# Performance work log

Hardware: AMD Instinct MI355X
Metric: run time of the kernel (lower is better)

The kernel has to match this reference:

```python
import jax, jax.numpy as jnp
import numpy as np

N_NODES = 100000
N_EDGES = 1600000
D_FEAT = 50
N_CLASSES = 47
K_HOPS = 2


def setup_inputs() -> dict:
    key = jax.random.key(0)
    k1, k2, k3, k4 = jax.random.split(key, 4)
    feat = jax.random.normal(k1, (N_NODES, D_FEAT), dtype=jnp.float32)
    edge_src = jax.random.randint(k2, (N_EDGES,), 0, N_NODES)
    edge_dst = jax.random.randint(k3, (N_EDGES,), 0, N_NODES)
    # xavier_uniform for fc.weight [n_classes, in_feats], zeros bias
    limit = np.sqrt(6.0 / (N_CLASSES + D_FEAT)).astype(np.float32)
    W = jax.random.uniform(k4, (N_CLASSES, D_FEAT), dtype=jnp.float32,
                           minval=-limit, maxval=limit)
    b = jnp.zeros((N_CLASSES,), dtype=jnp.float32)
    return {"feat": feat, "W": W, "b": b,
            "edge_src": edge_src, "edge_dst": edge_dst, "K": K_HOPS}


def reference(feat, W, b, edge_src, edge_dst, K):
    # S = D^-1/2 (A + I) D^-1/2 ; precompute = S^K ; out = (S^K feat) W^T + b
    N = feat.shape[0]
    ones = jnp.ones_like(edge_dst, dtype=feat.dtype)
    deg = 1.0 + jax.ops.segment_sum(ones, edge_dst, num_segments=N)  # row sums of A+I
    dinv = jax.lax.rsqrt(deg)                       # [N]
    w_e = dinv[edge_dst] * dinv[edge_src]           # [E] edge weights of S
    self_w = dinv * dinv                            # [N] self-loop weights (1/d)
    h = feat
    for _ in range(K):  # K hops: h <- S @ h
        msg = w_e[:, None] * h[edge_src]            # [E, D] gather + scale
        h = jax.ops.segment_sum(msg, edge_dst, num_segments=N) + self_w[:, None] * h
    return h @ W.T + b                              # [N, n_classes]
```

## Files before the change

### kernel.cpp

```cpp
#include <hip/hip_runtime.h>
#include <hip/hip_fp16.h>

#define NN 100000
#define NE 1600000
#define DF 50
#define NC 47
#define DP 64
#define ZROW NN
#define MAXDEG 48

#define RB   128
#define RSH  7
#define RNG  782
#define CCH  250
#define CI4  (NE / 4 / CCH)
#define BK   48

static_assert(NN % 16 == 0, "grid exactness");
static_assert((NE / 4) % CCH == 0, "chunk exactness");

typedef _Float16 half8 __attribute__((ext_vector_type(8)));
typedef float float4v __attribute__((ext_vector_type(4)));
typedef int int4v __attribute__((ext_vector_type(4)));

__global__ __launch_bounds__(256) void binA_kernel(const int4v* __restrict__ src4,
                                                   const int4v* __restrict__ dst4,
                                                   unsigned* __restrict__ arena,
                                                   unsigned short* __restrict__ counts) {
    __shared__ unsigned lcnt[RNG];
    int c = blockIdx.x;
    for (int i = threadIdx.x; i < RNG; i += 256) lcnt[i] = 0;
    __syncthreads();
    int base = c * CI4;
    for (int i = threadIdx.x; i < CI4; i += 256) {
        int4v s = __builtin_nontemporal_load(&src4[base + i]);
        int4v q = __builtin_nontemporal_load(&dst4[base + i]);
        #pragma unroll
        for (int k = 0; k < 4; ++k) {
            unsigned d  = (unsigned)q[k];
            unsigned r  = d >> RSH;
            unsigned dl = d & (RB - 1);
            unsigned p  = atomicAdd(&lcnt[r], 1u);
            if (p < BK)
                arena[((size_t)r * CCH + c) * BK + p] = (unsigned)s[k] | (dl << 17);
        }
    }
    __syncthreads();
    for (int i = threadIdx.x; i < RNG; i += 256)
        counts[(size_t)c * RNG + i] = (unsigned short)min(lcnt[i], (unsigned)BK);
}

__global__ __launch_bounds__(256) void slotB_kernel(const unsigned* __restrict__ arena,
                                                    const unsigned short* __restrict__ counts,
                                                    int* __restrict__ cols,
                                                    unsigned* __restrict__ deg) {
    __shared__ unsigned lcur[RB];
    int r = blockIdx.x;
    if (threadIdx.x < RB) lcur[threadIdx.x] = 0;
    __syncthreads();
    int c = threadIdx.x;
    if (c < CCH) {
        int cnt = counts[(size_t)c * RNG + r];
        const unsigned* bk = arena + ((size_t)r * CCH + c) * BK;
        for (int j = 0; j < cnt; ++j) {
            unsigned e    = bk[j];
            unsigned srcv = e & 0x1FFFFu;
            unsigned dl   = (e >> 17) & (RB - 1);
            unsigned p    = atomicAdd(&lcur[dl], 1u);
            if (p < MAXDEG)
                cols[((size_t)r * RB + dl) * MAXDEG + p] = (int)srcv;
        }
    }
    __syncthreads();
    if (threadIdx.x < RB) {
        int node = r * RB + threadIdx.x;
        if (node < NN) deg[node] = lcur[threadIdx.x];
    }
}

__global__ void pad_kernel(const unsigned* __restrict__ deg, const float* __restrict__ f,
                           float* __restrict__ dinv, float* __restrict__ selfw,
                           float4* __restrict__ fp, float4* __restrict__ h1p4) {
    int t = blockIdx.x * blockDim.x + threadIdx.x;
    if (t >= (NN + 1) * 8) return;
    int n = t >> 3, c = t & 7;
    float r = 0.f;
    if (n < NN) r = rsqrtf(1.0f + (float)deg[n]);
    if (c == 0 && n < NN) {
        dinv[n]  = r;
        selfw[n] = r * r;
    }
    float v[8];
    #pragma unroll
    for (int i = 0; i < 8; ++i) {
        int e = c * 8 + i;
        v[i] = (n < NN && e < DF) ? r * f[n * DF + e] : 0.f;
    }
    float4 ov;
    __half2* op = (__half2*)&ov;
    #pragma unroll
    for (int i = 0; i < 4; ++i) op[i] = __floats2half2_rn(v[2 * i], v[2 * i + 1]);
    fp[t] = ov;
    if (n == NN) h1p4[t] = make_float4(0.f, 0.f, 0.f, 0.f);
}

__global__ __launch_bounds__(256) void hop_kernel(const _Float16* __restrict__ h,
    const int* __restrict__ cols, const unsigned* __restrict__ deg,
    const float* __restrict__ scaleArr, _Float16* __restrict__ hn) {

    int lane = threadIdx.x & 63;
    int wid  = (int)((blockIdx.x * blockDim.x + threadIdx.x) >> 6);
    int half = lane >> 5;
    int g    = (lane >> 3) & 3;
    int qid  = lane & 7;

    int nd = 2 * wid + half;
    unsigned rs = (unsigned)nd * MAXDEG;
    unsigned d  = min(deg[nd], (unsigned)MAXDEG);
    unsigned dmax = max(__shfl(d, 0), __shfl(d, 32));

    float acc[8] = {0.f, 0.f, 0.f, 0.f, 0.f, 0.f, 0.f, 0.f};

    auto body = [&](unsigned j) {
        int c = __builtin_nontemporal_load(&cols[rs + j]);
        c = (j < d) ? c : ZROW;
        half8 v = *(const half8*)(h + (unsigned)c * DP + qid * 8);
        #pragma unroll
        for (int i = 0; i < 8; ++i) acc[i] += (float)v[i];
    };

    for (unsigned j0 = 0; j0 < dmax; j0 += 32u) {
        #pragma unroll
        for (int u = 0; u < 4; ++u) body(j0 + (unsigned)(g + 4 * u));
        if (j0 + 16u < dmax) {
            #pragma unroll
            for (int u = 4; u < 8; ++u) body(j0 + (unsigned)(g + 4 * u));
        }
    }

    #pragma unroll
    for (int i = 0; i < 8; ++i) {
        acc[i] += __shfl_xor(acc[i], 8);
        acc[i] += __shfl_xor(acc[i], 16);
    }

    float s = scaleArr[nd];
    half8 hv = *(const half8*)(h + (unsigned)nd * DP + qid * 8);
    half8 ov;
    #pragma unroll
    for (int i = 0; i < 8; ++i)
        ov[i] = (_Float16)(s * (acc[i] + (float)hv[i]));
    if ((lane & 24) == 0)
        __builtin_nontemporal_store(ov, (half8*)(hn + (unsigned)nd * DP + qid * 8));
}

__global__ __launch_bounds__(256) void fc_kernel(const _Float16* __restrict__ h2,
    const float* __restrict__ W, const float* __restrict__ b,
    float* __restrict__ out, int MT) {

    __shared__ _Float16 sW[48 * 72];
    __shared__ float sB[48];

    for (int i = threadIdx.x; i < 48 * 64; i += 256) {
        int n = i >> 6, k = i & 63;
        float v = (n < NC && k < DF) ? W[n * DF + k] : 0.f;
        sW[n * 72 + k] = (_Float16)v;
    }
    if (threadIdx.x < 48) sB[threadIdx.x] = (threadIdx.x < NC) ? b[threadIdx.x] : 0.f;
    __syncthreads();

    int lane = threadIdx.x & 63;
    int wid  = (int)((blockIdx.x * blockDim.x + threadIdx.x) >> 6);
    if (wid >= MT) return;

    int m0 = wid * 16;
    int am = lane & 15;
    int aq = lane >> 4;

    const half8* arow = (const half8*)(h2 + (long)(m0 + am) * DP);
    half8 a0 = arow[aq];
    half8 a1 = arow[aq + 4];
    int row = aq * 4;

    #pragma unroll
    for (int t = 0; t < 3; ++t) {
        int n = t * 16 + am;
        const half8* brow = (const half8*)(sW + n * 72);
        half8 b0 = brow[aq];
        half8 b1 = brow[aq + 4];
        float4v c = {0.f, 0.f, 0.f, 0.f};
        c = __builtin_amdgcn_mfma_f32_16x16x32_f16(a0, b0, c, 0, 0, 0);
        c = __builtin_amdgcn_mfma_f32_16x16x32_f16(a1, b1, c, 0, 0, 0);
        if (n < NC) {
            float bn = sB[n];
            #pragma unroll
            for (int r = 0; r < 4; ++r)
                out[(long)(m0 + row + r) * NC + n] = c[r] + bn;
        }
    }
}

extern "C" void kernel_launch(void* const* d_in, const int* in_sizes, int n_in,
                              void* d_out, int out_size, void* d_ws, size_t ws_size,
                              hipStream_t stream) {
    const float* feat = (const float*)d_in[0];
    const float* W    = (const float*)d_in[1];
    const float* b    = (const float*)d_in[2];
    const int*  esrc  = (const int*)d_in[3];
    const int*  edst  = (const int*)d_in[4];
    float* out = (float*)d_out;

    char* ws = (char*)d_ws;
    unsigned* deg    = (unsigned*)ws;       ws += ((size_t)NN * 4 + 127) & ~127ull;
    float*    dinv   = (float*)ws;          ws += ((size_t)NN * 4 + 127) & ~127ull;
    float*    selfw  = (float*)ws;          ws += ((size_t)NN * 4 + 127) & ~127ull;
    int*      cols   = (int*)ws;            ws += ((size_t)NN * MAXDEG * 4 + 127) & ~127ull;
    unsigned short* counts = (unsigned short*)ws; ws += ((size_t)CCH * RNG * 2 + 127) & ~127ull;
    char* uni = ws;
    unsigned* arena  = (unsigned*)uni;
    _Float16* featp  = (_Float16*)uni;
    _Float16* h1p    = featp + (size_t)(NN + 1) * DP;
    _Float16* h2p    = h1p   + (size_t)(NN + 1) * DP;

    binA_kernel<<<CCH, 256, 0, stream>>>((const int4v*)esrc, (const int4v*)edst, arena, counts);
    slotB_kernel<<<RNG, 256, 0, stream>>>(arena, counts, cols, deg);

    pad_kernel<<<((NN + 1) * 8 + 255) / 256, 256, 0, stream>>>(
        deg, feat, dinv, selfw, (float4*)featp, (float4*)h1p);

    const int hop_blocks = NN / 8;
    hop_kernel<<<hop_blocks, 256, 0, stream>>>(featp, cols, deg, selfw, h1p);
    hop_kernel<<<hop_blocks, 256, 0, stream>>>(h1p, cols, deg, dinv, h2p);

    const int MT = NN / 16;
    fc_kernel<<<(MT + 3) / 4, 256, 0, stream>>>(h2p, W, b, out, MT);
}
```

Before: 220.8 us.

## Apply linear layer before propagation and fuse bias into final hop

Reorders the computation to (S^K X W^T) so the dense projection runs first on raw features, folding the dinv scaling and padding into the projection kernel. The second hop now writes the final fp32 output with bias directly, which removes the separate pad and fc kernels and the h2 intermediate buffer. The binning stage also doubles the chunk count and halves the per-bucket capacity, which changes the parallelism of the edge-binning pass. Risks are fp16 rounding of the projected features and bucket overflow, which silently drops edges, now that the per-bucket cap is smaller.

After: 223.7 us. About the same (+1.3%).

```diff
diff --git a/kernel.cpp b/kernel.cpp
--- a/kernel.cpp
+++ b/kernel.cpp
@@ -12,9 +12,9 @@
 #define RB   128
 #define RSH  7
 #define RNG  782
-#define CCH  250
+#define CCH  500
 #define CI4  (NE / 4 / CCH)
-#define BK   48
+#define BK   24
 
 static_assert(NN % 16 == 0, "grid exactness");
 static_assert((NE / 4) % CCH == 0, "chunk exactness");
@@ -58,8 +58,7 @@
     int r = blockIdx.x;
     if (threadIdx.x < RB) lcur[threadIdx.x] = 0;
     __syncthreads();
-    int c = threadIdx.x;
-    if (c < CCH) {
+    for (int c = threadIdx.x; c < CCH; c += 256) {
         int cnt = counts[(size_t)c * RNG + r];
         const unsigned* bk = arena + ((size_t)r * CCH + c) * BK;
         for (int j = 0; j < cnt; ++j) {
@@ -78,109 +77,50 @@
     }
 }
 
-__global__ void pad_kernel(const unsigned* __restrict__ deg, const float* __restrict__ f,
-                           float* __restrict__ dinv, float* __restrict__ selfw,
-                           float4* __restrict__ fp, float4* __restrict__ h1p4) {
-    int t = blockIdx.x * blockDim.x + threadIdx.x;
-    if (t >= (NN + 1) * 8) return;
-    int n = t >> 3, c = t & 7;
-    float r = 0.f;
-    if (n < NN) r = rsqrtf(1.0f + (float)deg[n]);
-    if (c == 0 && n < NN) {
-        dinv[n]  = r;
-        selfw[n] = r * r;
-    }
-    float v[8];
-    #pragma unroll
-    for (int i = 0; i < 8; ++i) {
-        int e = c * 8 + i;
-        v[i] = (n < NN && e < DF) ? r * f[n * DF + e] : 0.f;
-    }
-    float4 ov;
-    __half2* op = (__half2*)&ov;
-    #pragma unroll
-    for (int i = 0; i < 4; ++i) op[i] = __floats2half2_rn(v[2 * i], v[2 * i + 1]);
-    fp[t] = ov;
-    if (n == NN) h1p4[t] = make_float4(0.f, 0.f, 0.f, 0.f);
-}
-
-__global__ __launch_bounds__(256) void hop_kernel(const _Float16* __restrict__ h,
-    const int* __restrict__ cols, const unsigned* __restrict__ deg,
-    const float* __restrict__ scaleArr, _Float16* __restrict__ hn) {
-
-    int lane = threadIdx.x & 63;
-    int wid  = (int)((blockIdx.x * blockDim.x + threadIdx.x) >> 6);
-    int half = lane >> 5;
-    int g    = (lane >> 3) & 3;
-    int qid  = lane & 7;
-
-    int nd = 2 * wid + half;
-    unsigned rs = (unsigned)nd * MAXDEG;
-    unsigned d  = min(deg[nd], (unsigned)MAXDEG);
-    unsigned dmax = max(__shfl(d, 0), __shfl(d, 32));
-
-    float acc[8] = {0.f, 0.f, 0.f, 0.f, 0.f, 0.f, 0.f, 0.f};
-
-    auto body = [&](unsigned j) {
-        int c = __builtin_nontemporal_load(&cols[rs + j]);
-        c = (j < d) ? c : ZROW;
-        half8 v = *(const half8*)(h + (unsigned)c * DP + qid * 8);
-        #pragma unroll
-        for (int i = 0; i < 8; ++i) acc[i] += (float)v[i];
-    };
-
-    for (unsigned j0 = 0; j0 < dmax; j0 += 32u) {
-        #pragma unroll
-        for (int u = 0; u < 4; ++u) body(j0 + (unsigned)(g + 4 * u));
-        if (j0 + 16u < dmax) {
-            #pragma unroll
-            for (int u = 4; u < 8; ++u) body(j0 + (unsigned)(g + 4 * u));
-        }
-    }
-
-    #pragma unroll
-    for (int i = 0; i < 8; ++i) {
-        acc[i] += __shfl_xor(acc[i], 8);
-        acc[i] += __shfl_xor(acc[i], 16);
-    }
-
-    float s = scaleArr[nd];
-    half8 hv = *(const half8*)(h + (unsigned)nd * DP + qid * 8);
-    half8 ov;
-    #pragma unroll
-    for (int i = 0; i < 8; ++i)
-        ov[i] = (_Float16)(s * (acc[i] + (float)hv[i]));
-    if ((lane & 24) == 0)
-        __builtin_nontemporal_store(ov, (half8*)(hn + (unsigned)nd * DP + qid * 8));
-}
-
-__global__ __launch_bounds__(256) void fc_kernel(const _Float16* __restrict__ h2,
-    const float* __restrict__ W, const float* __restrict__ b,
-    float* __restrict__ out, int MT) {
-
+__global__ __launch_bounds__(256) void yw_kernel(const float* __restrict__ feat,
+                                                 const unsigned* __restrict__ deg,
+                                                 const float* __restrict__ W,
+                                                 _Float16* __restrict__ Y,
+                                                 _Float16* __restrict__ h1p, int MT) {
     __shared__ _Float16 sW[48 * 72];
-    __shared__ float sB[48];
+    __shared__ _Float16 sY[4][16][72];
 
     for (int i = threadIdx.x; i < 48 * 64; i += 256) {
         int n = i >> 6, k = i & 63;
         float v = (n < NC && k < DF) ? W[n * DF + k] : 0.f;
         sW[n * 72 + k] = (_Float16)v;
     }
-    if (threadIdx.x < 48) sB[threadIdx.x] = (threadIdx.x < NC) ? b[threadIdx.x] : 0.f;
     __syncthreads();
 
     int lane = threadIdx.x & 63;
-    int wid  = (int)((blockIdx.x * blockDim.x + threadIdx.x) >> 6);
-    if (wid >= MT) return;
+    int w    = threadIdx.x >> 6;
+    int wid  = blockIdx.x * 4 + w;
+    if (wid > MT) return;
+    if (wid == MT) {
+        half8 z = {};
+        if (lane < 8)       *(half8*)(Y   + (size_t)ZROW * DP + lane * 8) = z;
+        else if (lane < 16) *(half8*)(h1p + (size_t)ZROW * DP + (lane - 8) * 8) = z;
+        return;
+    }
 
     int m0 = wid * 16;
     int am = lane & 15;
     int aq = lane >> 4;
-
-    const half8* arow = (const half8*)(h2 + (long)(m0 + am) * DP);
-    half8 a0 = arow[aq];
-    half8 a1 = arow[aq + 4];
     int row = aq * 4;
+
+    const float* arow = feat + (size_t)(m0 + am) * DF;
+    half8 a0, a1;
+    #pragma unroll
+    for (int j = 0; j < 8; ++j) {
+        a0[j] = (_Float16)arow[aq * 8 + j];
+        int k1 = 32 + aq * 8 + j;
+        a1[j] = (k1 < DF) ? (_Float16)arow[k1] : (_Float16)0.f;
+    }
+
+    float dv[4];
+    #pragma unroll
+    for (int r = 0; r < 4; ++r)
+        dv[r] = rsqrtf(1.0f + (float)deg[m0 + row + r]);
 
     #pragma unroll
     for (int t = 0; t < 3; ++t) {
@@ -191,11 +131,103 @@
         float4v c = {0.f, 0.f, 0.f, 0.f};
         c = __builtin_amdgcn_mfma_f32_16x16x32_f16(a0, b0, c, 0, 0, 0);
         c = __builtin_amdgcn_mfma_f32_16x16x32_f16(a1, b1, c, 0, 0, 0);
-        if (n < NC) {
-            float bn = sB[n];
+        #pragma unroll
+        for (int r = 0; r < 4; ++r)
+            sY[w][row + r][n] = (_Float16)(c[r] * dv[r]);
+    }
+    #pragma unroll
+    for (int r = 0; r < 4; ++r)
+        sY[w][row + r][48 + am] = (_Float16)0.f;
+
+    int row2 = lane >> 2, q = lane & 3;
+    half8 y0 = *(half8*)&sY[w][row2][q * 16];
+    half8 y1 = *(half8*)&sY[w][row2][q * 16 + 8];
+    _Float16* orow = Y + (size_t)(m0 + row2) * DP + q * 16;
+    *(half8*)orow = y0;
+    *(half8*)(orow + 8) = y1;
+}
+
+__device__ __forceinline__ void gather_sum(const _Float16* __restrict__ h,
+    const int* __restrict__ cols, unsigned rs, unsigned d, unsigned dmax,
+    int qid, int g, float* acc) {
+    auto body = [&](unsigned j) {
+        int c = __builtin_nontemporal_load(&cols[rs + j]);
+        c = (j < d) ? c : ZROW;
+        half8 v = *(const half8*)(h + (unsigned)c * DP + qid * 8);
+        #pragma unroll
+        for (int i = 0; i < 8; ++i) acc[i] += (float)v[i];
+    };
+    for (unsigned j0 = 0; j0 < dmax; j0 += 32u) {
+        #pragma unroll
+        for (int u = 0; u < 4; ++u) body(j0 + (unsigned)(g + 4 * u));
+        if (j0 + 16u < dmax) {
             #pragma unroll
-            for (int r = 0; r < 4; ++r)
-                out[(long)(m0 + row + r) * NC + n] = c[r] + bn;
+            for (int u = 4; u < 8; ++u) body(j0 + (unsigned)(g + 4 * u));
+        }
+    }
+    #pragma unroll
+    for (int i = 0; i < 8; ++i) {
+        acc[i] += __shfl_xor(acc[i], 8);
+        acc[i] += __shfl_xor(acc[i], 16);
+    }
+}
+
+__global__ __launch_bounds__(256) void hop1_kernel(const _Float16* __restrict__ h,
+    const int* __restrict__ cols, const unsigned* __restrict__ deg,
+    _Float16* __restrict__ hn) {
+
+    int lane = threadIdx.x & 63;
+    int wid  = (int)((blockIdx.x * blockDim.x + threadIdx.x) >> 6);
+    int half = lane >> 5, g = (lane >> 3) & 3, qid = lane & 7;
+
+    int nd = 2 * wid + half;
+    unsigned du = deg[nd];
+    unsigned d  = min(du, (unsigned)MAXDEG);
+    unsigned dmax = max(__shfl(d, 0), __shfl(d, 32));
+    unsigned rs = (unsigned)nd * MAXDEG;
+
+    float acc[8] = {0.f, 0.f, 0.f, 0.f, 0.f, 0.f, 0.f, 0.f};
+    gather_sum(h, cols, rs, d, dmax, qid, g, acc);
+
+    float s = 1.0f / (1.0f + (float)du);
+    half8 hv = *(const half8*)(h + (unsigned)nd * DP + qid * 8);
+    half8 ov;
+    #pragma unroll
+    for (int i = 0; i < 8; ++i)
+        ov[i] = (_Float16)(s * (acc[i] + (float)hv[i]));
+    if ((lane & 24) == 0)
+        __builtin_nontemporal_store(ov, (half8*)(hn + (unsigned)nd * DP + qid * 8));
+}
+
+__global__ __launch_bounds__(256) void hop2_kernel(const _Float16* __restrict__ h,
+    const int* __restrict__ cols, const unsigned* __restrict__ deg,
+    const float* __restrict__ bias, float* __restrict__ out) {
+
+    __shared__ float sB[64];
+    if (threadIdx.x < 64) sB[threadIdx.x] = (threadIdx.x < NC) ? bias[threadIdx.x] : 0.f;
+    __syncthreads();
+
+    int lane = threadIdx.x & 63;
+    int wid  = (int)((blockIdx.x * blockDim.x + threadIdx.x) >> 6);
+    int half = lane >> 5, g = (lane >> 3) & 3, qid = lane & 7;
+
+    int nd = 2 * wid + half;
+    unsigned du = deg[nd];
+    unsigned d  = min(du, (unsigned)MAXDEG);
+    unsigned dmax = max(__shfl(d, 0), __shfl(d, 32));
+    unsigned rs = (unsigned)nd * MAXDEG;
+
+    float acc[8] = {0.f, 0.f, 0.f, 0.f, 0.f, 0.f, 0.f, 0.f};
+    gather_sum(h, cols, rs, d, dmax, qid, g, acc);
+
+    float s = rsqrtf(1.0f + (float)du);
+    half8 hv = *(const half8*)(h + (unsigned)nd * DP + qid * 8);
+    if ((lane & 24) == 0) {
+        #pragma unroll
+        for (int i = 0; i < 8; ++i) {
+            int cidx = qid * 8 + i;
+            if (cidx < NC)
+                out[(size_t)nd * NC + cidx] = s * (acc[i] + (float)hv[i]) + sB[cidx];
         }
     }
 }
@@ -212,26 +244,20 @@
 
     char* ws = (char*)d_ws;
     unsigned* deg    = (unsigned*)ws;       ws += ((size_t)NN * 4 + 127) & ~127ull;
-    float*    dinv   = (float*)ws;          ws += ((size_t)NN * 4 + 127) & ~127ull;
-    float*    selfw  = (float*)ws;          ws += ((size_t)NN * 4 + 127) & ~127ull;
     int*      cols   = (int*)ws;            ws += ((size_t)NN * MAXDEG * 4 + 127) & ~127ull;
     unsigned short* counts = (unsigned short*)ws; ws += ((size_t)CCH * RNG * 2 + 127) & ~127ull;
     char* uni = ws;
     unsigned* arena  = (unsigned*)uni;
-    _Float16* featp  = (_Float16*)uni;
-    _Float16* h1p    = featp + (size_t)(NN + 1) * DP;
-    _Float16* h2p    = h1p   + (size_t)(NN + 1) * DP;
+    _Float16* Y      = (_Float16*)uni;
+    _Float16* h1p    = Y + (size_t)(NN + 1) * DP;
 
     binA_kernel<<<CCH, 256, 0, stream>>>((const int4v*)esrc, (const int4v*)edst, arena, counts);
     slotB_kernel<<<RNG, 256, 0, stream>>>(arena, counts, cols, deg);
 
-    pad_kernel<<<((NN + 1) * 8 + 255) / 256, 256, 0, stream>>>(
-        deg, feat, dinv, selfw, (float4*)featp, (float4*)h1p);
+    const int MT = NN / 16;
+    yw_kernel<<<(MT + 1 + 3) / 4, 256, 0, stream>>>(feat, deg, W, Y, h1p, MT);
 
     const int hop_blocks = NN / 8;
-    hop_kernel<<<hop_blocks, 256, 0, stream>>>(featp, cols, deg, selfw, h1p);
-    hop_kernel<<<hop_blocks, 256, 0, stream>>>(h1p, cols, deg, dinv, h2p);
-
-    const int MT = NN / 16;
-    fc_kernel<<<(MT + 3) / 4, 256, 0, stream>>>(h2p, W, b, out, MT);
-}
+    hop1_kernel<<<hop_blocks, 256, 0, stream>>>(Y,   cols, deg, h1p);
+    hop2_kernel<<<hop_blocks, 256, 0, stream>>>(h1p, cols, deg, b, out);
+}
```
